# Kernel optimization log

Hardware: AMD Instinct MI355X
Metric: run time of the kernel (lower is better)

Reference implementation:

```python
import jax, jax.numpy as jnp
import numpy as np

B, S, D, H = 4, 2048, 1024, 16
HD = D // H

def setup_inputs() -> dict:
    key = jax.random.key(0)
    ks = jax.random.split(key, 5)
    s = 1.0 / np.sqrt(D)
    return {
        "x": jax.random.normal(ks[0], (B, S, D), dtype=jnp.float32),
        "Wq": jax.random.normal(ks[1], (D, D), dtype=jnp.float32) * s,
        "Wk": jax.random.normal(ks[2], (D, D), dtype=jnp.float32) * s,
        "Wv": jax.random.normal(ks[3], (D, D), dtype=jnp.float32) * s,
        "Wo": jax.random.normal(ks[4], (D, D), dtype=jnp.float32) * s,
        "bo": jnp.zeros((D,), dtype=jnp.float32),
    }

def reference(x, Wq, Wk, Wv, Wo, bo):
    b, n, _ = x.shape
    # torch Linear: x @ W.T ; split heads -> [b, h, n, hd]
    def proj(W):
        return (x @ W.T).reshape(b, n, H, HD).transpose(0, 2, 1, 3)
    q, k, v = proj(Wq), proj(Wk), proj(Wv)
    scores = jnp.einsum('bhqd,bhkd->bhqk', q, k)  # [b,h,n,n]
    causal = jnp.triu(jnp.ones((n, n), dtype=bool), k=1)
    scores = jnp.where(causal, -jnp.inf, scores)
    attn = jax.nn.softmax(scores / np.sqrt(HD), axis=-1)  # dropout p=0.0 (eval)
    ctx = jnp.einsum('bhqk,bhkd->bhqd', attn, v)
    ctx = ctx.transpose(0, 2, 1, 3).reshape(b, n, D)
    return ctx @ Wo.T + bo
```

## Files before the change

### kernel.cpp

```cpp
#include <hip/hip_runtime.h>
#include <stdint.h>
#include <cmath>

#define BATCH 4
#define SEQ   2048
#define DM    1024
#define NH    16
#define HDIM  64
#define MROWS (BATCH*SEQ)
#define NQB   16

typedef __attribute__((ext_vector_type(8)))  __bf16 bf16x8;
typedef __attribute__((ext_vector_type(8)))  unsigned short u16x8;
typedef __attribute__((ext_vector_type(4)))  float f32x4;
typedef __attribute__((ext_vector_type(16))) float f32x16;
typedef __attribute__((ext_vector_type(4)))  unsigned int u32x4;

__device__ __forceinline__ unsigned short f2bf(float f) {
  unsigned u = __float_as_uint(f);
  u = (u + 0x7FFFu + ((u >> 16) & 1u)) >> 16;
  return (unsigned short)u;
}

__device__ __forceinline__ f32x4 mfma_bf16(bf16x8 a, bf16x8 b, f32x4 c) {
  return __builtin_amdgcn_mfma_f32_16x16x32_bf16(a, b, c, 0, 0, 0);
}
__device__ __forceinline__ f32x16 mfma32(bf16x8 a, bf16x8 b, f32x16 c) {
  return __builtin_amdgcn_mfma_f32_32x32x16_bf16(a, b, c, 0, 0, 0);
}

__device__ __forceinline__ unsigned cvtpk(float lo, float hi) {
  unsigned r;
  asm("v_cvt_pk_bf16_f32 %0, %1, %2" : "=v"(r) : "v"(lo), "v"(hi));
  return r;
}
__device__ __forceinline__ void permswap(unsigned &a, unsigned &b) {
  asm volatile("v_permlane32_swap_b32 %0, %1" : "+v"(a), "+v"(b));
}
__device__ __forceinline__ f32x16 zero16() {
  f32x16 z;
#pragma unroll
  for (int i = 0; i < 16; ++i) z[i] = 0.f;
  return z;
}

typedef const __attribute__((address_space(1))) unsigned int* as1_u32p;
typedef __attribute__((address_space(3))) unsigned int* as3_u32p;

__device__ __forceinline__ void gload16(const void* g, void* l) {
  __builtin_amdgcn_global_load_lds((as1_u32p)g, (as3_u32p)l, 16, 0, 0);
}

__global__ void cvt_f32_bf16(const float* __restrict__ src,
                             unsigned short* __restrict__ dst, int n4) {
  int i = blockIdx.x * blockDim.x + threadIdx.x;
  int stride = gridDim.x * blockDim.x;
  for (; i < n4; i += stride) {
    float4 v = ((const float4*)src)[i];
    ushort4 o;
    o.x = f2bf(v.x); o.y = f2bf(v.y); o.z = f2bf(v.z); o.w = f2bf(v.w);
    ((ushort4*)dst)[i] = o;
  }
}

__global__ void cvt_w4(const float* __restrict__ s0, const float* __restrict__ s1,
                       const float* __restrict__ s2, const float* __restrict__ s3,
                       unsigned short* __restrict__ d0, unsigned short* __restrict__ d1,
                       unsigned short* __restrict__ d2, unsigned short* __restrict__ d3,
                       int n4) {
  const float* src = (blockIdx.y == 0) ? s0 : (blockIdx.y == 1) ? s1 : (blockIdx.y == 2) ? s2 : s3;
  unsigned short* dst = (blockIdx.y == 0) ? d0 : (blockIdx.y == 1) ? d1 : (blockIdx.y == 2) ? d2 : d3;
  int i = blockIdx.x * blockDim.x + threadIdx.x;
  int stride = gridDim.x * blockDim.x;
  for (; i < n4; i += stride) {
    float4 v = ((const float4*)src)[i];
    ushort4 o;
    o.x = f2bf(v.x); o.y = f2bf(v.y); o.z = f2bf(v.z); o.w = f2bf(v.w);
    ((ushort4*)dst)[i] = o;
  }
}

__device__ __forceinline__ void gemm_tile_mainloop(
    const unsigned short* __restrict__ A, const unsigned short* __restrict__ Bw,
    int rowBase, int colBase,
    unsigned short* As, unsigned short* Bs,
    f32x4 acc[4][4], int tid)
{
  const int wid = tid >> 6, lane = tid & 63;
  const int wm = wid >> 1, wn = wid & 1;
  const unsigned short* Atile = A + (size_t)rowBase * DM;
  const unsigned short* Btile = Bw + (size_t)colBase * DM;

  for (int k0 = 0; k0 < DM; k0 += 64) {
#pragma unroll
    for (int j = 0; j < 4; ++j) {
      int c = j * 256 + tid;
      int row = c >> 3;
      int inB = (c & 7) * 16;
      int srcE = row * DM + k0 + ((inB ^ ((row & 7) << 4)) >> 1);
      gload16(Atile + srcE, As + (size_t)(j * 256 + wid * 64) * 8);
    }
#pragma unroll
    for (int j = 0; j < 4; ++j) {
      int c = j * 256 + tid;
      int row = c >> 3;
      int inB = (c & 7) * 16;
      int srcE = row * DM + k0 + ((inB ^ ((row & 7) << 4)) >> 1);
      gload16(Btile + srcE, Bs + (size_t)(j * 256 + wid * 64) * 8);
    }
    __syncthreads();

#pragma unroll
    for (int s2 = 0; s2 < 2; ++s2) {
      bf16x8 af[4], bfv[4];
#pragma unroll
      for (int m = 0; m < 4; ++m) {
        int row = wm * 64 + m * 16 + (lane & 15);
        int off = row * 128 + ((s2 * 64 + ((lane >> 4) * 16)) ^ ((row & 7) << 4));
        af[m] = *(const bf16x8*)((const char*)As + off);
      }
#pragma unroll
      for (int n = 0; n < 4; ++n) {
        int row = wn * 64 + n * 16 + (lane & 15);
        int off = row * 128 + ((s2 * 64 + ((lane >> 4) * 16)) ^ ((row & 7) << 4));
        bfv[n] = *(const bf16x8*)((const char*)Bs + off);
      }
#pragma unroll
      for (int m = 0; m < 4; ++m)
#pragma unroll
        for (int n = 0; n < 4; ++n)
          acc[m][n] = mfma_bf16(af[m], bfv[n], acc[m][n]);
    }
    __syncthreads();
  }
}

__global__ __launch_bounds__(256, 2) void gemm_qkv(
    const unsigned short* __restrict__ xb,
    const unsigned short* __restrict__ Wqb, const unsigned short* __restrict__ Wkb,
    const unsigned short* __restrict__ Wvb,
    unsigned short* __restrict__ Qd, unsigned short* __restrict__ Kd,
    unsigned short* __restrict__ Vd)
{
  __shared__ unsigned short As[128 * 64];
  __shared__ unsigned short Bs[128 * 64];
  const int tid = threadIdx.x;
  const int z = blockIdx.z;
  const unsigned short* W = (z == 0) ? Wqb : (z == 1) ? Wkb : Wvb;
  unsigned short* dst = (z == 0) ? Qd : (z == 1) ? Kd : Vd;
  const int rowBase = blockIdx.x * 128, colBase = blockIdx.y * 128;

  f32x4 acc[4][4];
#pragma unroll
  for (int m = 0; m < 4; ++m)
#pragma unroll
    for (int n = 0; n < 4; ++n) acc[m][n] = (f32x4){0.f, 0.f, 0.f, 0.f};

  gemm_tile_mainloop(xb, W, rowBase, colBase, As, Bs, acc, tid);

  const int wid = tid >> 6, lane = tid & 63;
  const int wm = wid >> 1, wn = wid & 1;
#pragma unroll
  for (int m = 0; m < 4; ++m)
#pragma unroll
    for (int n = 0; n < 4; ++n)
#pragma unroll
      for (int r = 0; r < 4; ++r) {
        int grow = rowBase + wm * 64 + m * 16 + ((lane >> 4) * 4) + r;
        int gcol = colBase + wn * 64 + n * 16 + (lane & 15);
        int b = grow >> 11, s = grow & (SEQ - 1);
        int h = gcol >> 6, hd = gcol & 63;
        dst[(((size_t)(b * NH + h)) * SEQ + s) * HDIM + hd] = f2bf(acc[m][n][r]);
      }
}

__global__ __launch_bounds__(256, 2) void gemm_out(
    const unsigned short* __restrict__ ctx, const unsigned short* __restrict__ Wob,
    const float* __restrict__ bo, float* __restrict__ out)
{
  __shared__ unsigned short As[128 * 64];
  __shared__ unsigned short Bs[128 * 64];
  const int tid = threadIdx.x;
  const int rowBase = blockIdx.x * 128, colBase = blockIdx.y * 128;

  f32x4 acc[4][4];
#pragma unroll
  for (int m = 0; m < 4; ++m)
#pragma unroll
    for (int n = 0; n < 4; ++n) acc[m][n] = (f32x4){0.f, 0.f, 0.f, 0.f};

  gemm_tile_mainloop(ctx, Wob, rowBase, colBase, As, Bs, acc, tid);

  const int wid = tid >> 6, lane = tid & 63;
  const int wm = wid >> 1, wn = wid & 1;
#pragma unroll
  for (int m = 0; m < 4; ++m)
#pragma unroll
    for (int n = 0; n < 4; ++n)
#pragma unroll
      for (int r = 0; r < 4; ++r) {
        int grow = rowBase + wm * 64 + m * 16 + ((lane >> 4) * 4) + r;
        int gcol = colBase + wn * 64 + n * 16 + (lane & 15);
        out[(size_t)grow * DM + gcol] = acc[m][n][r] + bo[gcol];
      }
}

__global__ void transpose_v(const unsigned short* __restrict__ Vd,
                            unsigned short* __restrict__ VT)
{
  __shared__ unsigned short tile[64 * 72];
  const int tid = threadIdx.x;
  const int bh = blockIdx.y, s0 = blockIdx.x * 64;
  const unsigned short* src = Vd + (size_t)bh * SEQ * HDIM + (size_t)s0 * HDIM;
#pragma unroll
  for (int j = 0; j < 2; ++j) {
    int c = j * 256 + tid;
    int r = c >> 3, c0 = (c & 7) * 8;
    *(u16x8*)(tile + r * 72 + c0) = *(const u16x8*)(src + r * HDIM + c0);
  }
  __syncthreads();
  unsigned short* dst = VT + (size_t)bh * HDIM * SEQ + s0;
#pragma unroll
  for (int j = 0; j < 2; ++j) {
    int c = j * 256 + tid;
    int d = c >> 3, c0 = (c & 7) * 8;
    u16x8 v;
#pragma unroll
    for (int e = 0; e < 8; ++e) v[e] = tile[(c0 + e) * 72 + d];
    *(u16x8*)(dst + (size_t)d * SEQ + c0) = v;
  }
}

__global__ __launch_bounds__(256, 2) void attn_fwd3(
    const unsigned short* __restrict__ Qg, const unsigned short* __restrict__ Kg,
    const unsigned short* __restrict__ VTg, unsigned short* __restrict__ ctx)
{
  __shared__ unsigned short smem[24576];

  const int tid = threadIdx.x, wid = tid >> 6, lane = tid & 63;
  const int hi = lane >> 5, lq = lane & 31;
  const int bh = blockIdx.y;
  const unsigned short* Qp = Qg  + (size_t)bh * SEQ * HDIM;
  const unsigned short* Kp = Kg  + (size_t)bh * SEQ * HDIM;
  const unsigned short* Vp = VTg + (size_t)bh * HDIM * SEQ;
  const int b = bh >> 4, h = bh & 15;

  auto stageK = [&](int t, int buf) {
#pragma unroll
    for (int j = 0; j < 2; ++j) {
      int c = j * 256 + tid;
      int row = c >> 3, inB = (c & 7) * 16;
      gload16(Kp + (size_t)(t * 64 + row) * HDIM + ((inB ^ ((row & 7) << 4)) >> 1),
              smem + buf * 4096 + (size_t)(j * 256 + wid * 64) * 8);
    }
  };
  auto stageV = [&](int t, int buf) {
#pragma unroll
    for (int j = 0; j < 2; ++j) {
      int c = j * 256 + tid;
      int row = c >> 3, inB = (c & 7) * 16;
      gload16(Vp + (size_t)row * SEQ + t * 64 + ((inB ^ ((row & 7) << 4)) >> 1),
              smem + 12288 + buf * 4096 + (size_t)(j * 256 + wid * 64) * 8);
    }
  };

  for (int half = 0; half < 2; ++half) {
    const int qb = half == 0 ? (int)blockIdx.x : (NQB - 1 - (int)blockIdx.x);
    const int qw0 = qb * 128 + wid * 32;

    bf16x8 qf[4];
    {
      const unsigned short* qrow = Qp + (size_t)(qw0 + lq) * HDIM + hi * 8;
#pragma unroll
      for (int ks = 0; ks < 4; ++ks) qf[ks] = *(const bf16x8*)(qrow + ks * 16);
    }

    f32x16 o0 = zero16(), o1 = zero16();
    float m_run = -INFINITY, l_run = 0.f;
    const int nt = 2 * qb + 2;

    stageK(0, 0); stageV(0, 0);
    stageK(1, 1); stageV(1, 1);
    asm volatile("s_waitcnt vmcnt(4)" ::: "memory");
    __builtin_amdgcn_s_barrier();

    for (int t = 0; t < nt; ++t) {
      const int cur = t % 3;
      const bool pf = (t + 2) < nt;
      if (pf) { int nb = (t + 2) % 3; stageK(t + 2, nb); stageV(t + 2, nb); }

      if (t * 64 <= qw0 + 31) {
        const unsigned short* Kl = smem + cur * 4096;
        f32x16 s0 = zero16(), s1 = zero16();
        __builtin_amdgcn_s_setprio(1);
#pragma unroll
        for (int ks = 0; ks < 4; ++ks) {
          int r0 = lq, r1 = lq + 32;
          int col = (ks * 32 + hi * 16);
          bf16x8 a0 = *(const bf16x8*)((const char*)Kl + r0 * 128 + (col ^ ((r0 & 7) << 4)));
          bf16x8 a1 = *(const bf16x8*)((const char*)Kl + r1 * 128 + (col ^ ((r1 & 7) << 4)));
          s0 = mfma32(a0, qf[ks], s0);
          s1 = mfma32(a1, qf[ks], s1);
        }
        __builtin_amdgcn_s_setprio(0);

        if (t * 64 + 63 > qw0) {
          const int q = qw0 + lq;
          const int kb = t * 64 + 4 * hi;
#pragma unroll
          for (int r = 0; r < 16; ++r) {
            int k0 = kb + (r & 3) + 8 * (r >> 2);
            if (k0 > q)      s0[r] = -INFINITY;
            if (k0 + 32 > q) s1[r] = -INFINITY;
          }
        }

        float pmax = s0[0];
#pragma unroll
        for (int r = 1; r < 16; ++r) pmax = fmaxf(pmax, s0[r]);
#pragma unroll
        for (int r = 0; r < 16; ++r) pmax = fmaxf(pmax, s1[r]);
        pmax = fmaxf(pmax, __shfl_xor(pmax, 32, 64));

        if (!__all(pmax - m_run <= 64.0f)) {
          float mn = fmaxf(m_run, pmax);
          float alpha = __expf((m_run - mn) * 0.125f);
          l_run *= alpha;
#pragma unroll
          for (int r = 0; r < 16; ++r) { o0[r] *= alpha; o1[r] *= alpha; }
          m_run = mn;
        }

        float rsum = 0.f;
#pragma unroll
        for (int r = 0; r < 16; ++r) {
          s0[r] = __expf((s0[r] - m_run) * 0.125f); rsum += s0[r];
        }
#pragma unroll
        for (int r = 0; r < 16; ++r) {
          s1[r] = __expf((s1[r] - m_run) * 0.125f); rsum += s1[r];
        }
        rsum += __shfl_xor(rsum, 32, 64);
        l_run += rsum;

        bf16x8 pfr[4];
#pragma unroll
        for (int h2 = 0; h2 < 2; ++h2) {
          {
            unsigned va = cvtpk(s0[h2 * 8 + 0], s0[h2 * 8 + 1]);
            unsigned vb = cvtpk(s0[h2 * 8 + 4], s0[h2 * 8 + 5]);
            unsigned vc = cvtpk(s0[h2 * 8 + 2], s0[h2 * 8 + 3]);
            unsigned vd = cvtpk(s0[h2 * 8 + 6], s0[h2 * 8 + 7]);
            permswap(va, vb); permswap(vc, vd);
            u32x4 tt; tt.x = va; tt.y = vc; tt.z = vb; tt.w = vd;
            pfr[h2] = __builtin_bit_cast(bf16x8, tt);
          }
          {
            unsigned va = cvtpk(s1[h2 * 8 + 0], s1[h2 * 8 + 1]);
            unsigned vb = cvtpk(s1[h2 * 8 + 4], s1[h2 * 8 + 5]);
            unsigned vc = cvtpk(s1[h2 * 8 + 2], s1[h2 * 8 + 3]);
            unsigned vd = cvtpk(s1[h2 * 8 + 6], s1[h2 * 8 + 7]);
            permswap(va, vb); permswap(vc, vd);
            u32x4 tt; tt.x = va; tt.y = vc; tt.z = vb; tt.w = vd;
            pfr[2 + h2] = __builtin_bit_cast(bf16x8, tt);
          }
        }

        const unsigned short* Vl = smem + 12288 + cur * 4096;
        __builtin_amdgcn_s_setprio(1);
#pragma unroll
        for (int ks = 0; ks < 4; ++ks) {
          int r0 = lq, r1 = lq + 32;
          int col = (ks * 32 + hi * 16);
          bf16x8 va0 = *(const bf16x8*)((const char*)Vl + r0 * 128 + (col ^ ((r0 & 7) << 4)));
          bf16x8 va1 = *(const bf16x8*)((const char*)Vl + r1 * 128 + (col ^ ((r1 & 7) << 4)));
          o0 = mfma32(va0, pfr[ks], o0);
          o1 = mfma32(va1, pfr[ks], o1);
        }
        __builtin_amdgcn_s_setprio(0);
      }

      if (pf) asm volatile("s_waitcnt vmcnt(4)" ::: "memory");
      else    asm volatile("s_waitcnt vmcnt(0)" ::: "memory");
      __builtin_amdgcn_s_barrier();
    }

    const float invl = 1.0f / l_run;
    unsigned short* Ot = smem;
    const int q = wid * 32 + lq;
#pragma unroll
    for (int r2 = 0; r2 < 16; r2 += 2) {
      int d = (r2 & 3) + 8 * (r2 >> 2) + 4 * hi;
      unsigned w0 = cvtpk(o0[r2] * invl, o0[r2 + 1] * invl);
      *(unsigned*)((char*)Ot + q * 128 + ((2 * d) ^ ((q & 7) << 4))) = w0;
      int d2 = d + 32;
      unsigned w1 = cvtpk(o1[r2] * invl, o1[r2 + 1] * invl);
      *(unsigned*)((char*)Ot + q * 128 + ((2 * d2) ^ ((q & 7) << 4))) = w1;
    }
    __syncthreads();

#pragma unroll
    for (int i = 0; i < 4; ++i) {
      int idx = i * 256 + tid;
      int qq = idx >> 3, c16 = (idx & 7) * 8;
      bf16x8 v = *(const bf16x8*)((const char*)Ot + qq * 128 + ((2 * c16) ^ ((qq & 7) << 4)));
      *(bf16x8*)(ctx + ((size_t)(b * SEQ) + qb * 128 + qq) * DM + h * 64 + c16) = v;
    }
    __syncthreads();
  }
}

extern "C" void kernel_launch(void* const* d_in, const int* in_sizes, int n_in,
                              void* d_out, int out_size, void* d_ws, size_t ws_size,
                              hipStream_t stream)
{
  (void)in_sizes; (void)n_in; (void)out_size; (void)ws_size;
  const float* x  = (const float*)d_in[0];
  const float* Wq = (const float*)d_in[1];
  const float* Wk = (const float*)d_in[2];
  const float* Wv = (const float*)d_in[3];
  const float* Wo = (const float*)d_in[4];
  const float* bo = (const float*)d_in[5];
  float* out = (float*)d_out;

  char* ws = (char*)d_ws;
  unsigned short* xb  = (unsigned short*)(ws);
  unsigned short* Wqb = (unsigned short*)(ws + (size_t)16 * 1048576);
  unsigned short* Wkb = (unsigned short*)(ws + (size_t)18 * 1048576);
  unsigned short* Wvb = (unsigned short*)(ws + (size_t)20 * 1048576);
  unsigned short* Wob = (unsigned short*)(ws + (size_t)22 * 1048576);
  unsigned short* Qd  = (unsigned short*)(ws + (size_t)24 * 1048576);
  unsigned short* Kd  = (unsigned short*)(ws + (size_t)40 * 1048576);
  unsigned short* Vd  = (unsigned short*)(ws + (size_t)56 * 1048576);
  unsigned short* ctxb= (unsigned short*)(ws + (size_t)72 * 1048576);
  unsigned short* VT  = xb;

  cvt_f32_bf16<<<2048, 256, 0, stream>>>(x, xb, MROWS * DM / 4);
  cvt_w4<<<dim3(64, 4), 256, 0, stream>>>(Wq, Wk, Wv, Wo, Wqb, Wkb, Wvb, Wob, DM * DM / 4);

  gemm_qkv<<<dim3(MROWS / 128, DM / 128, 3), 256, 0, stream>>>(xb, Wqb, Wkb, Wvb, Qd, Kd, Vd);
  transpose_v<<<dim3(SEQ / 64, BATCH * NH), 256, 0, stream>>>(Vd, VT);
  attn_fwd3<<<dim3(NQB / 2, BATCH * NH), 256, 0, stream>>>(Qd, Kd, VT, ctxb);
  gemm_out<<<dim3(MROWS / 128, DM / 128, 1), 256, 0, stream>>>(ctxb, Wob, bo, out);
}
```

Before: 242.3 us.

## Double-buffer GEMM LDS tiles, use exp2 softmax, precompute attention addresses

The shared GEMM mainloop now double-buffers its A/B tiles in LDS, prefetching the next k-slice while MFMAs run on the current one, with precomputed source pointers. The attention kernel switches softmax to raw v_exp_f32 with a folded log2e*scale FMA, precomputes LDS read offsets and staging pointers, and uses a pairwise max reduction. This aims to hide global-load latency in the projection GEMMs and cut VALU work in the attention inner loop. Doubling GEMM LDS to 64KB per block may reduce occupancy, and the waitcnt(0) at the end of each iteration limits how much overlap the prefetch can give.

```diff
diff --git a/kernel.cpp b/kernel.cpp
--- a/kernel.cpp
+++ b/kernel.cpp
@@ -36,6 +36,11 @@
 }
 __device__ __forceinline__ void permswap(unsigned &a, unsigned &b) {
   asm volatile("v_permlane32_swap_b32 %0, %1" : "+v"(a), "+v"(b));
+}
+__device__ __forceinline__ float exp2v(float x) {
+  float r;
+  asm("v_exp_f32 %0, %1" : "=v"(r) : "v"(x));
+  return r;
 }
 __device__ __forceinline__ f32x16 zero16() {
   f32x16 z;
@@ -88,28 +93,44 @@
 {
   const int wid = tid >> 6, lane = tid & 63;
   const int wm = wid >> 1, wn = wid & 1;
-  const unsigned short* Atile = A + (size_t)rowBase * DM;
-  const unsigned short* Btile = Bw + (size_t)colBase * DM;
+
+  const unsigned short* aSrc[4];
+  const unsigned short* bSrc[4];
+  int ldsDst[4];
+#pragma unroll
+  for (int j = 0; j < 4; ++j) {
+    int c = j * 256 + tid;
+    int row = c >> 3;
+    int inB = (c & 7) * 16;
+    int off = row * DM + ((inB ^ ((row & 7) << 4)) >> 1);
+    aSrc[j] = A + (size_t)rowBase * DM + off;
+    bSrc[j] = Bw + (size_t)colBase * DM + off;
+    ldsDst[j] = (j * 256 + wid * 64) * 8;
+  }
+
+  auto stage = [&](int buf) {
+#pragma unroll
+    for (int j = 0; j < 4; ++j) {
+      gload16(aSrc[j], As + buf * 8192 + ldsDst[j]);
+      aSrc[j] += 64;
+    }
+#pragma unroll
+    for (int j = 0; j < 4; ++j) {
+      gload16(bSrc[j], Bs + buf * 8192 + ldsDst[j]);
+      bSrc[j] += 64;
+    }
+  };
+
+  stage(0);
+  asm volatile("s_waitcnt vmcnt(0)" ::: "memory");
+  __builtin_amdgcn_s_barrier();
 
   for (int k0 = 0; k0 < DM; k0 += 64) {
-#pragma unroll
-    for (int j = 0; j < 4; ++j) {
-      int c = j * 256 + tid;
-      int row = c >> 3;
-      int inB = (c & 7) * 16;
-      int srcE = row * DM + k0 + ((inB ^ ((row & 7) << 4)) >> 1);
-      gload16(Atile + srcE, As + (size_t)(j * 256 + wid * 64) * 8);
-    }
-#pragma unroll
-    for (int j = 0; j < 4; ++j) {
-      int c = j * 256 + tid;
-      int row = c >> 3;
-      int inB = (c & 7) * 16;
-      int srcE = row * DM + k0 + ((inB ^ ((row & 7) << 4)) >> 1);
-      gload16(Btile + srcE, Bs + (size_t)(j * 256 + wid * 64) * 8);
-    }
-    __syncthreads();
-
+    const int cur = (k0 >> 6) & 1;
+    if (k0 + 64 < DM) stage(cur ^ 1);
+
+    const char* Ab = (const char*)As + cur * 16384;
+    const char* Bb = (const char*)Bs + cur * 16384;
 #pragma unroll
     for (int s2 = 0; s2 < 2; ++s2) {
       bf16x8 af[4], bfv[4];
@@ -117,13 +138,13 @@
       for (int m = 0; m < 4; ++m) {
         int row = wm * 64 + m * 16 + (lane & 15);
         int off = row * 128 + ((s2 * 64 + ((lane >> 4) * 16)) ^ ((row & 7) << 4));
-        af[m] = *(const bf16x8*)((const char*)As + off);
+        af[m] = *(const bf16x8*)(Ab + off);
       }
 #pragma unroll
       for (int n = 0; n < 4; ++n) {
         int row = wn * 64 + n * 16 + (lane & 15);
         int off = row * 128 + ((s2 * 64 + ((lane >> 4) * 16)) ^ ((row & 7) << 4));
-        bfv[n] = *(const bf16x8*)((const char*)Bs + off);
+        bfv[n] = *(const bf16x8*)(Bb + off);
       }
 #pragma unroll
       for (int m = 0; m < 4; ++m)
@@ -131,7 +152,8 @@
         for (int n = 0; n < 4; ++n)
           acc[m][n] = mfma_bf16(af[m], bfv[n], acc[m][n]);
     }
-    __syncthreads();
+    asm volatile("s_waitcnt vmcnt(0)" ::: "memory");
+    __builtin_amdgcn_s_barrier();
   }
 }
 
@@ -142,8 +164,8 @@
     unsigned short* __restrict__ Qd, unsigned short* __restrict__ Kd,
     unsigned short* __restrict__ Vd)
 {
-  __shared__ unsigned short As[128 * 64];
-  __shared__ unsigned short Bs[128 * 64];
+  __shared__ unsigned short As[2 * 128 * 64];
+  __shared__ unsigned short Bs[2 * 128 * 64];
   const int tid = threadIdx.x;
   const int z = blockIdx.z;
   const unsigned short* W = (z == 0) ? Wqb : (z == 1) ? Wkb : Wvb;
@@ -178,8 +200,8 @@
     const unsigned short* __restrict__ ctx, const unsigned short* __restrict__ Wob,
     const float* __restrict__ bo, float* __restrict__ out)
 {
-  __shared__ unsigned short As[128 * 64];
-  __shared__ unsigned short Bs[128 * 64];
+  __shared__ unsigned short As[2 * 128 * 64];
+  __shared__ unsigned short Bs[2 * 128 * 64];
   const int tid = threadIdx.x;
   const int rowBase = blockIdx.x * 128, colBase = blockIdx.y * 128;
 
@@ -244,30 +266,48 @@
   const unsigned short* Kp = Kg  + (size_t)bh * SEQ * HDIM;
   const unsigned short* Vp = VTg + (size_t)bh * HDIM * SEQ;
   const int b = bh >> 4, h = bh & 15;
-
-  auto stageK = [&](int t, int buf) {
-#pragma unroll
-    for (int j = 0; j < 2; ++j) {
-      int c = j * 256 + tid;
-      int row = c >> 3, inB = (c & 7) * 16;
-      gload16(Kp + (size_t)(t * 64 + row) * HDIM + ((inB ^ ((row & 7) << 4)) >> 1),
-              smem + buf * 4096 + (size_t)(j * 256 + wid * 64) * 8);
-    }
-  };
-  auto stageV = [&](int t, int buf) {
-#pragma unroll
-    for (int j = 0; j < 2; ++j) {
-      int c = j * 256 + tid;
-      int row = c >> 3, inB = (c & 7) * 16;
-      gload16(Vp + (size_t)row * SEQ + t * 64 + ((inB ^ ((row & 7) << 4)) >> 1),
-              smem + 12288 + buf * 4096 + (size_t)(j * 256 + wid * 64) * 8);
-    }
-  };
+  const float C2 = 0.18033688f;
+
+  int sRow[2], sSwz[2], sDst[2];
+#pragma unroll
+  for (int j = 0; j < 2; ++j) {
+    int c = j * 256 + tid;
+    sRow[j] = c >> 3;
+    sSwz[j] = (((c & 7) * 16) ^ ((sRow[j] & 7) << 4)) >> 1;
+    sDst[j] = (j * 256 + wid * 64) * 8;
+  }
+  int off0[4], off1[4];
+#pragma unroll
+  for (int ks = 0; ks < 4; ++ks) {
+    int col = ks * 32 + hi * 16;
+    off0[ks] = lq * 128 + (col ^ ((lq & 7) << 4));
+    off1[ks] = (lq + 32) * 128 + (col ^ ((lq & 7) << 4));
+  }
 
   for (int half = 0; half < 2; ++half) {
     const int qb = half == 0 ? (int)blockIdx.x : (NQB - 1 - (int)blockIdx.x);
     const int qw0 = qb * 128 + wid * 32;
 
+    const unsigned short* kSrc[2];
+    const unsigned short* vSrc[2];
+#pragma unroll
+    for (int j = 0; j < 2; ++j) {
+      kSrc[j] = Kp + (size_t)sRow[j] * HDIM + sSwz[j];
+      vSrc[j] = Vp + (size_t)sRow[j] * SEQ + sSwz[j];
+    }
+    auto stageKV = [&](int buf) {
+#pragma unroll
+      for (int j = 0; j < 2; ++j) {
+        gload16(kSrc[j], smem + buf * 4096 + sDst[j]);
+        kSrc[j] += 64 * HDIM;
+      }
+#pragma unroll
+      for (int j = 0; j < 2; ++j) {
+        gload16(vSrc[j], smem + 12288 + buf * 4096 + sDst[j]);
+        vSrc[j] += 64;
+      }
+    };
+
     bf16x8 qf[4];
     {
       const unsigned short* qrow = Qp + (size_t)(qw0 + lq) * HDIM + hi * 8;
@@ -276,29 +316,26 @@
     }
 
     f32x16 o0 = zero16(), o1 = zero16();
-    float m_run = -INFINITY, l_run = 0.f;
+    float m_run = -INFINITY, l_run = 0.f, mc2 = 0.f;
     const int nt = 2 * qb + 2;
 
-    stageK(0, 0); stageV(0, 0);
-    stageK(1, 1); stageV(1, 1);
+    stageKV(0); stageKV(1);
     asm volatile("s_waitcnt vmcnt(4)" ::: "memory");
     __builtin_amdgcn_s_barrier();
 
     for (int t = 0; t < nt; ++t) {
       const int cur = t % 3;
       const bool pf = (t + 2) < nt;
-      if (pf) { int nb = (t + 2) % 3; stageK(t + 2, nb); stageV(t + 2, nb); }
+      if (pf) stageKV((t + 2) % 3);
 
       if (t * 64 <= qw0 + 31) {
-        const unsigned short* Kl = smem + cur * 4096;
+        const char* Kl = (const char*)smem + cur * 8192;
         f32x16 s0 = zero16(), s1 = zero16();
         __builtin_amdgcn_s_setprio(1);
 #pragma unroll
         for (int ks = 0; ks < 4; ++ks) {
-          int r0 = lq, r1 = lq + 32;
-          int col = (ks * 32 + hi * 16);
-          bf16x8 a0 = *(const bf16x8*)((const char*)Kl + r0 * 128 + (col ^ ((r0 & 7) << 4)));
-          bf16x8 a1 = *(const bf16x8*)((const char*)Kl + r1 * 128 + (col ^ ((r1 & 7) << 4)));
+          bf16x8 a0 = *(const bf16x8*)(Kl + off0[ks]);
+          bf16x8 a1 = *(const bf16x8*)(Kl + off1[ks]);
           s0 = mfma32(a0, qf[ks], s0);
           s1 = mfma32(a1, qf[ks], s1);
         }
@@ -315,30 +352,33 @@
           }
         }
 
-        float pmax = s0[0];
-#pragma unroll
-        for (int r = 1; r < 16; ++r) pmax = fmaxf(pmax, s0[r]);
-#pragma unroll
-        for (int r = 0; r < 16; ++r) pmax = fmaxf(pmax, s1[r]);
+        float pmax = fmaxf(s0[0], s0[1]);
+#pragma unroll
+        for (int r = 2; r < 16; r += 2) pmax = fmaxf(pmax, fmaxf(s0[r], s0[r + 1]));
+#pragma unroll
+        for (int r = 0; r < 16; r += 2) pmax = fmaxf(pmax, fmaxf(s1[r], s1[r + 1]));
         pmax = fmaxf(pmax, __shfl_xor(pmax, 32, 64));
 
         if (!__all(pmax - m_run <= 64.0f)) {
           float mn = fmaxf(m_run, pmax);
-          float alpha = __expf((m_run - mn) * 0.125f);
+          float alpha = exp2v((m_run - mn) * C2);
           l_run *= alpha;
 #pragma unroll
           for (int r = 0; r < 16; ++r) { o0[r] *= alpha; o1[r] *= alpha; }
           m_run = mn;
+          mc2 = mn * C2;
         }
 
         float rsum = 0.f;
 #pragma unroll
         for (int r = 0; r < 16; ++r) {
-          s0[r] = __expf((s0[r] - m_run) * 0.125f); rsum += s0[r];
+          float p = exp2v(__builtin_fmaf(s0[r], C2, -mc2));
+          s0[r] = p; rsum += p;
         }
 #pragma unroll
         for (int r = 0; r < 16; ++r) {
-          s1[r] = __expf((s1[r] - m_run) * 0.125f); rsum += s1[r];
+          float p = exp2v(__builtin_fmaf(s1[r], C2, -mc2));
+          s1[r] = p; rsum += p;
         }
         rsum += __shfl_xor(rsum, 32, 64);
         l_run += rsum;
@@ -366,14 +406,12 @@
           }
         }
 
-        const unsigned short* Vl = smem + 12288 + cur * 4096;
+        const char* Vl = (const char*)smem + 24576 + cur * 8192;
         __builtin_amdgcn_s_setprio(1);
 #pragma unroll
         for (int ks = 0; ks < 4; ++ks) {
-          int r0 = lq, r1 = lq + 32;
-          int col = (ks * 32 + hi * 16);
-          bf16x8 va0 = *(const bf16x8*)((const char*)Vl + r0 * 128 + (col ^ ((r0 & 7) << 4)));
-          bf16x8 va1 = *(const bf16x8*)((const char*)Vl + r1 * 128 + (col ^ ((r1 & 7) << 4)));
+          bf16x8 va0 = *(const bf16x8*)(Vl + off0[ks]);
+          bf16x8 va1 = *(const bf16x8*)(Vl + off1[ks]);
           o0 = mfma32(va0, pfr[ks], o0);
           o1 = mfma32(va1, pfr[ks], o1);
         }
```

Result: slower. 253.6 us (+4.7%).
